# Performance work log

Measured on AMD Instinct MI355X. Metric: run time of the kernel, lower is better.

## Reference

```python
import jax, jax.numpy as jnp
import numpy as np

N_NODES = 50000
N_EDGES = 800000
N_FEAT = 128
HIDDEN = 256
N_CLASSES = 40
K_HOPS = 10
ALPHA = 0.1


def setup_inputs() -> dict:
    key = jax.random.key(0)
    k1, k2, k3, k4 = jax.random.split(key, 4)
    x = jax.random.normal(k1, (N_NODES, N_FEAT), dtype=jnp.float32)
    edge_index = jax.random.randint(k2, (2, N_EDGES), 0, N_NODES, dtype=jnp.int64)
    # PPR init of gamma weights: temp[k] = alpha*(1-alpha)^k, temp[K] = (1-alpha)^K
    temp_np = ALPHA * (1.0 - ALPHA) ** np.arange(K_HOPS + 1)
    temp_np[-1] = (1.0 - ALPHA) ** K_HOPS
    temp = jnp.asarray(temp_np, dtype=jnp.float32)
    W1 = jax.random.normal(k3, (N_FEAT, HIDDEN), dtype=jnp.float32) * (1.0 / np.sqrt(N_FEAT))
    b1 = jnp.zeros((HIDDEN,), dtype=jnp.float32)
    W2 = jax.random.normal(k4, (HIDDEN, N_CLASSES), dtype=jnp.float32) * (1.0 / np.sqrt(HIDDEN))
    b2 = jnp.zeros((N_CLASSES,), dtype=jnp.float32)
    return {"x": x, "edge_index": edge_index, "temp": temp,
            "W1": W1, "b1": b1, "W2": W2, "b2": b2, "K": K_HOPS}


def reference(x, edge_index, temp, W1, b1, W2, b2, K):
    N = x.shape[0]
    # gcn_norm with self-loops (fill value 1): A_hat = D^-1/2 (A + I) D^-1/2
    loops = jnp.arange(N, dtype=edge_index.dtype)
    row = jnp.concatenate([edge_index[0], loops])  # source (x_j)
    col = jnp.concatenate([edge_index[1], loops])  # target (aggregation)
    ones = jnp.ones(row.shape[0], dtype=x.dtype)
    deg = jax.ops.segment_sum(ones, col, num_segments=N)
    dinv = jnp.where(deg > 0, deg ** -0.5, jnp.zeros_like(deg))
    norm = dinv[row] * dinv[col]  # [E+N]

    # K-hop propagation with learned hop-weighted sum
    h = x
    hidden = temp[0] * x
    for k in range(K):  # small fixed hop count
        msg = norm[:, None] * h[row]                      # gather + scale
        h = jax.ops.segment_sum(msg, col, num_segments=N)  # scatter-add
        hidden = hidden + temp[k + 1] * h

    # eval mode: dropout is a no-op
    z = jax.nn.relu(hidden @ W1 + b1)
    z = z @ W2 + b2
    return jax.nn.log_softmax(z, axis=1)
```

## Files before the change

### kernel.cpp

```cpp
#include <hip/hip_runtime.h>
#include <hip/hip_bf16.h>


#define NFEAT 128
#define HID   256
#define NCLS  40
#define KHOPS 10

typedef __attribute__((ext_vector_type(8))) short short8;
typedef __attribute__((ext_vector_type(4))) float floatx4;

__device__ __forceinline__ float blo(unsigned g) { return __uint_as_float(g << 16); }
__device__ __forceinline__ float bhi(unsigned g) { return __uint_as_float(g & 0xffff0000u); }
__device__ __forceinline__ unsigned f2bf(float x) {
  unsigned u = __float_as_uint(x);
  return (u + 0x7fffu + ((u >> 16) & 1u)) >> 16;
}
__device__ __forceinline__ unsigned bpack(float a, float b) {
  return f2bf(a) | (f2bf(b) << 16);
}

__global__ void k_detect64(const unsigned int* __restrict__ raw, int* __restrict__ flag) {
  __shared__ int any;
  int t = threadIdx.x;
  if (t == 0) any = 0;
  __syncthreads();
  if (raw[2 * t + 1] != 0u) any = 1;
  __syncthreads();
  if (t == 0) flag[0] = (any == 0) ? 1 : 0;
}

__global__ void k_zero(int* __restrict__ p, int n) {
  int i = blockIdx.x * blockDim.x + threadIdx.x;
  if (i < n) p[i] = 0;
}

__global__ void k_count(const int* __restrict__ ei32, const long long* __restrict__ ei64,
                        int E, int N, int* __restrict__ cnt, int* __restrict__ rank,
                        const int* __restrict__ flag) {
  int e = blockIdx.x * blockDim.x + threadIdx.x;
  if (e >= E) return;
  int dst = flag[0] ? (int)ei64[(size_t)E + e] : ei32[(size_t)E + e];
  if ((unsigned)dst < (unsigned)N) rank[e] = atomicAdd(&cnt[dst], 1);
  else rank[e] = -1;
}

__global__ __launch_bounds__(256) void k_scan_a(
    const int* __restrict__ cnt, int* __restrict__ bsum, int n) {
  int t = threadIdx.x;
  int base = blockIdx.x * 1024 + t * 4;
  int s = 0;
  if (base + 3 < n) {
    int4 v = *(const int4*)(cnt + base);
    s = v.x + v.y + v.z + v.w;
  } else {
    #pragma unroll
    for (int j = 0; j < 4; ++j) if (base + j < n) s += cnt[base + j];
  }
  #pragma unroll
  for (int off = 1; off < 64; off <<= 1) s += __shfl_xor(s, off);
  __shared__ int ws[4];
  if ((t & 63) == 0) ws[t >> 6] = s;
  __syncthreads();
  if (t == 0) bsum[blockIdx.x] = ws[0] + ws[1] + ws[2] + ws[3];
}

__global__ void k_scan_mid(int* __restrict__ bsum, int* __restrict__ S,
                           int ntiles, int n) {
  int t = threadIdx.x;
  int lane = t & 63, wid = t >> 6;
  int v = (t < ntiles) ? bsum[t] : 0;
  int x = v;
  #pragma unroll
  for (int off = 1; off < 64; off <<= 1) {
    int u = __shfl_up(x, off);
    if (lane >= off) x += u;
  }
  __shared__ int ws[16];
  if (lane == 63) ws[wid] = x;
  __syncthreads();
  if (wid == 0) {
    int s2 = (lane < 16) ? ws[lane] : 0;
    #pragma unroll
    for (int off = 1; off < 16; off <<= 1) {
      int u = __shfl_up(s2, off);
      if (lane >= off) s2 += u;
    }
    if (lane < 16) ws[lane] = s2;
  }
  __syncthreads();
  int woff = wid ? ws[wid - 1] : 0;
  if (t < ntiles) bsum[t] = x - v + woff;
  if (t == 0) S[n] = ws[15];
}

__global__ __launch_bounds__(256) void k_scan_c(
    const int* __restrict__ cnt, const int* __restrict__ bsum,
    int* __restrict__ S, float* __restrict__ dinv, int n) {
  int t = threadIdx.x;
  int base = blockIdx.x * 1024 + t * 4;
  int v[4];
  if (base + 3 < n) {
    int4 q = *(const int4*)(cnt + base);
    v[0] = q.x; v[1] = q.y; v[2] = q.z; v[3] = q.w;
  } else {
    #pragma unroll
    for (int j = 0; j < 4; ++j) v[j] = (base + j < n) ? cnt[base + j] : 0;
  }
  int tsum = v[0] + v[1] + v[2] + v[3];
  int lane = t & 63, wv = t >> 6;
  int x = tsum;
  #pragma unroll
  for (int off = 1; off < 64; off <<= 1) {
    int u = __shfl_up(x, off);
    if (lane >= off) x += u;
  }
  __shared__ int ws[4];
  if (lane == 63) ws[wv] = x;
  __syncthreads();
  int woff = 0;
  #pragma unroll
  for (int j = 0; j < 4; ++j) if (j < wv) woff += ws[j];
  int run = x - tsum + woff + bsum[blockIdx.x];
  #pragma unroll
  for (int j = 0; j < 4; ++j) {
    int idx = base + j;
    if (idx < n) {
      S[idx] = run;
      dinv[idx] = rsqrtf((float)(v[j] + 1));
      run += v[j];
    }
  }
}

__global__ void k_fill(const int* __restrict__ ei32, const long long* __restrict__ ei64,
                       int E, int N, const int* __restrict__ S,
                       const int* __restrict__ rank, int* __restrict__ csr,
                       const int* __restrict__ flag) {
  int e = blockIdx.x * blockDim.x + threadIdx.x;
  if (e >= E) return;
  int r = rank[e];
  if (r < 0) return;
  int src, dst;
  if (flag[0]) { src = (int)ei64[e]; dst = (int)ei64[(size_t)E + e]; }
  else         { src = ei32[e];      dst = ei32[(size_t)E + e]; }
  if ((unsigned)src >= (unsigned)N) return;
  csr[S[dst] + r] = src;
}

__global__ void k_init(const float* __restrict__ x, const float* __restrict__ dinv,
                       unsigned* __restrict__ p0, int total64) {
  int i = blockIdx.x * blockDim.x + threadIdx.x;
  if (i >= total64) return;
  float2 xv = ((const float2*)x)[i];
  float di = dinv[i >> 6];
  p0[i] = bpack(di * xv.x, di * xv.y);
}

__global__ __launch_bounds__(256) void k_prop(
    const unsigned* __restrict__ pin, unsigned* __restrict__ pout,
    const int* __restrict__ S, const int* __restrict__ csr,
    const float* __restrict__ dinv, int N) {
  int wid = __builtin_amdgcn_readfirstlane(threadIdx.x >> 6);
  int lane = threadIdx.x & 63;
  int node = blockIdx.x * 4 + wid;
  if (node >= N) return;
  int g = lane & 15;
  int e = lane >> 4;
  int s = S[node], en = S[node + 1];
  float acc[8] = {0.f, 0.f, 0.f, 0.f, 0.f, 0.f, 0.f, 0.f};
  for (int p = s; p < en; p += 16) {
    uint4 gd[4];
    float wt[4];
    #pragma unroll
    for (int t = 0; t < 4; ++t) {
      int pj = p + t * 4 + e;
      int sidx = csr[pj < en ? pj : s];
      wt[t] = (pj < en) ? 1.f : 0.f;
      gd[t] = *(const uint4*)(pin + (size_t)sidx * 64 + g * 4);
    }
    #pragma unroll
    for (int t = 0; t < 4; ++t) {
      const unsigned* gu = (const unsigned*)&gd[t];
      #pragma unroll
      for (int u = 0; u < 4; ++u) {
        acc[u * 2]     += wt[t] * blo(gu[u]);
        acc[u * 2 + 1] += wt[t] * bhi(gu[u]);
      }
    }
  }
  #pragma unroll
  for (int u = 0; u < 8; ++u) {
    acc[u] += __shfl_xor(acc[u], 16);
    acc[u] += __shfl_xor(acc[u], 32);
  }
  if (e == 0) {
    float di = dinv[node];
    float dd = di * di;
    uint4 gs = *(const uint4*)(pin + (size_t)node * 64 + g * 4);
    const unsigned* su = (const unsigned*)&gs;
    #pragma unroll
    for (int u = 0; u < 4; ++u) {
      acc[u * 2]     += blo(su[u]);
      acc[u * 2 + 1] += bhi(su[u]);
    }
    uint4 pk;
    pk.x = bpack(dd * acc[0], dd * acc[1]);
    pk.y = bpack(dd * acc[2], dd * acc[3]);
    pk.z = bpack(dd * acc[4], dd * acc[5]);
    pk.w = bpack(dd * acc[6], dd * acc[7]);
    *(uint4*)(pout + (size_t)node * 64 + g * 4) = pk;
  }
}

__global__ __launch_bounds__(256) void k_gemm1f(
    const unsigned* __restrict__ pbuf, const float* __restrict__ temp,
    const float* __restrict__ dinv, const float* __restrict__ W1,
    const float* __restrict__ b1, unsigned short* __restrict__ z1, int M) {
  __shared__ unsigned short As[64][136];
  __shared__ unsigned short Bs[16][128][8];
  int tid = threadIdx.x;
  int m0 = blockIdx.x * 64;
  size_t slab = (size_t)M * 64;
  float tk[KHOPS + 1];
  #pragma unroll
  for (int k = 0; k <= KHOPS; ++k) tk[k] = temp[k];
  for (int idx = tid; idx < 64 * 16; idx += 256) {
    int m = idx >> 4, c = idx & 15;
    int row = m0 + m; if (row >= M) row = M - 1;
    const unsigned* pp = pbuf + (size_t)row * 64 + c * 4;
    float tL[4] = {0.f, 0.f, 0.f, 0.f}, tH[4] = {0.f, 0.f, 0.f, 0.f};
    #pragma unroll
    for (int k = 0; k <= KHOPS; ++k) {
      uint4 v = *(const uint4*)(pp + slab * k);
      const unsigned* vu = (const unsigned*)&v;
      #pragma unroll
      for (int u = 0; u < 4; ++u) {
        tL[u] += tk[k] * blo(vu[u]);
        tH[u] += tk[k] * bhi(vu[u]);
      }
    }
    float inv = 1.f / dinv[row];
    uint4 o;
    o.x = bpack(tL[0] * inv, tH[0] * inv);
    o.y = bpack(tL[1] * inv, tH[1] * inv);
    o.z = bpack(tL[2] * inv, tH[2] * inv);
    o.w = bpack(tL[3] * inv, tH[3] * inv);
    *(uint4*)&As[m][c * 8] = o;
  }
  __syncthreads();
  int lane = tid & 63;
  int q = lane >> 4, r16 = lane & 15;
  int nw = (tid >> 6) * 32;
  #pragma unroll
  for (int pass = 0; pass < 2; ++pass) {
    int n0 = pass * 128;
    if (pass) __syncthreads();
    for (int idx = tid; idx < 128 * 128; idx += 256) {
      int k = idx >> 7, n = idx & 127;
      Bs[k >> 3][n][k & 7] = (unsigned short)f2bf(W1[(size_t)k * HID + n0 + n]);
    }
    __syncthreads();
    floatx4 acc[4][2] = {};
    #pragma unroll
    for (int step = 0; step < 4; ++step) {
      int k0 = step * 32;
      short8 a[4], b[2];
      #pragma unroll
      for (int i = 0; i < 4; ++i)
        a[i] = *(const short8*)&As[i * 16 + r16][k0 + q * 8];
      #pragma unroll
      for (int j = 0; j < 2; ++j)
        b[j] = *(const short8*)&Bs[step * 4 + q][nw + j * 16 + r16][0];
      #pragma unroll
      for (int i = 0; i < 4; ++i)
        #pragma unroll
        for (int j = 0; j < 2; ++j)
          acc[i][j] = __builtin_amdgcn_mfma_f32_16x16x32_bf16(a[i], b[j], acc[i][j], 0, 0, 0);
    }
    __syncthreads();
    unsigned short* Zs = &Bs[0][0][0];
    #pragma unroll
    for (int j = 0; j < 2; ++j) {
      int n = nw + j * 16 + r16;
      float bias = b1[n0 + n];
      #pragma unroll
      for (int i = 0; i < 4; ++i) {
        #pragma unroll
        for (int r = 0; r < 4; ++r) {
          int m = i * 16 + q * 4 + r;
          float v = fmaxf(acc[i][j][r] + bias, 0.f);
          Zs[m * 136 + n] = (unsigned short)f2bf(v);
        }
      }
    }
    __syncthreads();
    for (int idx = tid; idx < 64 * 16; idx += 256) {
      int m = idx >> 4, c = idx & 15;
      int row = m0 + m;
      if (row < M) {
        uint4 v = *(const uint4*)&Zs[m * 136 + c * 8];
        *(uint4*)(z1 + (size_t)row * HID + n0 + c * 8) = v;
      }
    }
  }
}

__global__ void k_w2prep(const float* __restrict__ W2, unsigned short* __restrict__ W2t) {
  int i = blockIdx.x * blockDim.x + threadIdx.x;
  if (i >= 48 * 256) return;
  int n = i >> 8, k = i & 255;
  W2t[n * 256 + k] = (n < NCLS) ? (unsigned short)f2bf(W2[(size_t)k * NCLS + n]) : 0;
}

__global__ __launch_bounds__(256) void k_mlp2(
    const unsigned short* __restrict__ z1, const unsigned short* __restrict__ W2t,
    const float* __restrict__ b2, float* __restrict__ out, int N) {
  int tid = threadIdx.x;
  int lane = tid & 63;
  int wv = tid >> 6;
  int node0 = blockIdx.x * 64 + wv * 16;
  int q = lane >> 4, m = lane & 15;
  int arow = node0 + m; if (arow >= N) arow = N - 1;
  const unsigned short* aptr = z1 + (size_t)arow * HID + q * 8;
  const unsigned short* bptr = W2t + (size_t)m * HID + q * 8;
  floatx4 acc[3] = {};
  #pragma unroll
  for (int step = 0; step < 8; ++step) {
    short8 a = *(const short8*)(aptr + step * 32);
    #pragma unroll
    for (int j = 0; j < 3; ++j) {
      short8 b = *(const short8*)(bptr + (size_t)j * 16 * HID + step * 32);
      acc[j] = __builtin_amdgcn_mfma_f32_16x16x32_bf16(a, b, acc[j], 0, 0, 0);
    }
  }
  int c = m;
  bool v2 = (c < NCLS - 32);
  float bb0 = b2[c], bb1 = b2[c + 16];
  float bb2 = v2 ? b2[c + 32] : 0.f;
  #pragma unroll
  for (int r = 0; r < 4; ++r) {
    int node = node0 + q * 4 + r;
    float l0 = acc[0][r] + bb0;
    float l1 = acc[1][r] + bb1;
    float l2 = v2 ? (acc[2][r] + bb2) : -3.4e38f;
    float mx = fmaxf(fmaxf(l0, l1), l2);
    #pragma unroll
    for (int off = 1; off < 16; off <<= 1) mx = fmaxf(mx, __shfl_xor(mx, off));
    float sm = __expf(l0 - mx) + __expf(l1 - mx) + (v2 ? __expf(l2 - mx) : 0.f);
    #pragma unroll
    for (int off = 1; off < 16; off <<= 1) sm += __shfl_xor(sm, off);
    float lse = mx + __logf(sm);
    if (node < N) {
      float* op = out + (size_t)node * NCLS + c;
      op[0] = l0 - lse;
      op[16] = l1 - lse;
      if (v2) op[32] = l2 - lse;
    }
  }
}

extern "C" void kernel_launch(void* const* d_in, const int* in_sizes, int n_in,
                              void* d_out, int out_size, void* d_ws, size_t ws_size,
                              hipStream_t stream) {
  const float*     x    = (const float*)d_in[0];
  const int*       ei32 = (const int*)d_in[1];
  const long long* ei64 = (const long long*)d_in[1];
  const float*     temp = (const float*)d_in[2];
  const float*     W1   = (const float*)d_in[3];
  const float*     b1   = (const float*)d_in[4];
  const float*     W2   = (const float*)d_in[5];
  const float*     b2   = (const float*)d_in[6];
  float* out = (float*)d_out;

  int N = in_sizes[0] / NFEAT;
  int E = in_sizes[1] / 2;

  char* w = (char*)d_ws;
  auto carve = [&](size_t bytes) -> void* {
    void* p = (void*)w;
    w += (bytes + 255) & ~(size_t)255;
    return p;
  };
  int*      flag      = (int*)     carve(4);
  int*      cnt       = (int*)     carve((size_t)N * 4);
  int*      S         = (int*)     carve(((size_t)N + 1) * 4);
  float*    dinv      = (float*)   carve((size_t)N * 4);
  int*      bsum      = (int*)     carve(1024 * 4);
  unsigned short* W2t = (unsigned short*)carve(48 * 256 * 2);
  int*      rank      = (int*)     carve((size_t)E * 4);
  int*      csr       = (int*)     carve((size_t)E * 4);
  unsigned* pbuf      = (unsigned*)carve((size_t)(KHOPS + 1) * N * 64 * 4);
  unsigned short* z1  = (unsigned short*)carve((size_t)N * HID * 2);

  int ntiles = (N + 1023) / 1024;
  size_t slab = (size_t)N * 64;

  k_detect64<<<1, 256, 0, stream>>>((const unsigned int*)d_in[1], flag);
  k_zero<<<(N + 255) / 256, 256, 0, stream>>>(cnt, N);
  k_count<<<(E + 255) / 256, 256, 0, stream>>>(ei32, ei64, E, N, cnt, rank, flag);
  k_scan_a<<<ntiles, 256, 0, stream>>>(cnt, bsum, N);
  k_scan_mid<<<1, 1024, 0, stream>>>(bsum, S, ntiles, N);
  k_scan_c<<<ntiles, 256, 0, stream>>>(cnt, bsum, S, dinv, N);
  k_fill<<<(E + 255) / 256, 256, 0, stream>>>(ei32, ei64, E, N, S, rank, csr, flag);
  k_init<<<(N * 64 + 255) / 256, 256, 0, stream>>>(x, dinv, pbuf, N * 64);
  k_w2prep<<<48, 256, 0, stream>>>(W2, W2t);

  for (int k = 0; k < KHOPS; ++k) {
    k_prop<<<(N + 3) / 4, 256, 0, stream>>>(
        pbuf + slab * k, pbuf + slab * (k + 1), S, csr, dinv, N);
  }

  k_gemm1f<<<(N + 63) / 64, 256, 0, stream>>>(
      pbuf, temp, dinv, W1, b1, z1, N);
  k_mlp2<<<(N + 63) / 64, 256, 0, stream>>>(z1, W2t, b2, out, N);
}
```

Before: 488.9 us.

## Fuse hop-sum, first GEMM, second GEMM and log-softmax into one kernel

Merges the hop-weighted sum plus W1 GEMM kernel with the W2 GEMM and log-softmax kernel, so the bf16 hidden activations stay in shared memory and are never written to or reread from global memory. W1 is converted to transposed bf16 once in a new prep kernel. Each block no longer re-converts all of W1 into LDS; MFMA B operands now come straight from global W1t, with each wave covering 64 output columns in a single pass. The trade-off is more accumulator registers per thread, a declared occupancy target of 4 blocks, and B loads that depend on cache instead of LDS.

```diff
diff --git a/kernel.cpp b/kernel.cpp
--- a/kernel.cpp
+++ b/kernel.cpp
@@ -213,18 +213,33 @@
   }
 }
 
-__global__ __launch_bounds__(256) void k_gemm1f(
+__global__ void k_w1prep(const float* __restrict__ W1, unsigned short* __restrict__ W1t) {
+  int i = blockIdx.x * blockDim.x + threadIdx.x;
+  if (i >= 256 * 128) return;
+  int n = i >> 7, k = i & 127;
+  W1t[n * 128 + k] = (unsigned short)f2bf(W1[(size_t)k * HID + n]);
+}
+
+__global__ void k_w2prep(const float* __restrict__ W2, unsigned short* __restrict__ W2t) {
+  int i = blockIdx.x * blockDim.x + threadIdx.x;
+  if (i >= 48 * 256) return;
+  int n = i >> 8, k = i & 255;
+  W2t[n * 256 + k] = (n < NCLS) ? (unsigned short)f2bf(W2[(size_t)k * NCLS + n]) : 0;
+}
+
+__global__ __launch_bounds__(256, 4) void k_fused(
     const unsigned* __restrict__ pbuf, const float* __restrict__ temp,
-    const float* __restrict__ dinv, const float* __restrict__ W1,
-    const float* __restrict__ b1, unsigned short* __restrict__ z1, int M) {
-  __shared__ unsigned short As[64][136];
-  __shared__ unsigned short Bs[16][128][8];
+    const float* __restrict__ dinv, const unsigned short* __restrict__ W1t,
+    const float* __restrict__ b1, const unsigned short* __restrict__ W2t,
+    const float* __restrict__ b2, float* __restrict__ out, int M) {
+  __shared__ unsigned short sbuf[64 * 264];
   int tid = threadIdx.x;
   int m0 = blockIdx.x * 64;
   size_t slab = (size_t)M * 64;
   float tk[KHOPS + 1];
   #pragma unroll
   for (int k = 0; k <= KHOPS; ++k) tk[k] = temp[k];
+
   for (int idx = tid; idx < 64 * 16; idx += 256) {
     int m = idx >> 4, c = idx & 15;
     int row = m0 + m; if (row >= M) row = M - 1;
@@ -246,104 +261,73 @@
     o.y = bpack(tL[1] * inv, tH[1] * inv);
     o.z = bpack(tL[2] * inv, tH[2] * inv);
     o.w = bpack(tL[3] * inv, tH[3] * inv);
-    *(uint4*)&As[m][c * 8] = o;
-  }
-  __syncthreads();
-  int lane = tid & 63;
-  int q = lane >> 4, r16 = lane & 15;
-  int nw = (tid >> 6) * 32;
-  #pragma unroll
-  for (int pass = 0; pass < 2; ++pass) {
-    int n0 = pass * 128;
-    if (pass) __syncthreads();
-    for (int idx = tid; idx < 128 * 128; idx += 256) {
-      int k = idx >> 7, n = idx & 127;
-      Bs[k >> 3][n][k & 7] = (unsigned short)f2bf(W1[(size_t)k * HID + n0 + n]);
-    }
-    __syncthreads();
-    floatx4 acc[4][2] = {};
-    #pragma unroll
-    for (int step = 0; step < 4; ++step) {
-      int k0 = step * 32;
-      short8 a[4], b[2];
-      #pragma unroll
-      for (int i = 0; i < 4; ++i)
-        a[i] = *(const short8*)&As[i * 16 + r16][k0 + q * 8];
-      #pragma unroll
-      for (int j = 0; j < 2; ++j)
-        b[j] = *(const short8*)&Bs[step * 4 + q][nw + j * 16 + r16][0];
-      #pragma unroll
-      for (int i = 0; i < 4; ++i)
-        #pragma unroll
-        for (int j = 0; j < 2; ++j)
-          acc[i][j] = __builtin_amdgcn_mfma_f32_16x16x32_bf16(a[i], b[j], acc[i][j], 0, 0, 0);
-    }
-    __syncthreads();
-    unsigned short* Zs = &Bs[0][0][0];
-    #pragma unroll
-    for (int j = 0; j < 2; ++j) {
-      int n = nw + j * 16 + r16;
-      float bias = b1[n0 + n];
-      #pragma unroll
-      for (int i = 0; i < 4; ++i) {
-        #pragma unroll
-        for (int r = 0; r < 4; ++r) {
-          int m = i * 16 + q * 4 + r;
-          float v = fmaxf(acc[i][j][r] + bias, 0.f);
-          Zs[m * 136 + n] = (unsigned short)f2bf(v);
-        }
-      }
-    }
-    __syncthreads();
-    for (int idx = tid; idx < 64 * 16; idx += 256) {
-      int m = idx >> 4, c = idx & 15;
-      int row = m0 + m;
-      if (row < M) {
-        uint4 v = *(const uint4*)&Zs[m * 136 + c * 8];
-        *(uint4*)(z1 + (size_t)row * HID + n0 + c * 8) = v;
-      }
-    }
-  }
-}
-
-__global__ void k_w2prep(const float* __restrict__ W2, unsigned short* __restrict__ W2t) {
-  int i = blockIdx.x * blockDim.x + threadIdx.x;
-  if (i >= 48 * 256) return;
-  int n = i >> 8, k = i & 255;
-  W2t[n * 256 + k] = (n < NCLS) ? (unsigned short)f2bf(W2[(size_t)k * NCLS + n]) : 0;
-}
-
-__global__ __launch_bounds__(256) void k_mlp2(
-    const unsigned short* __restrict__ z1, const unsigned short* __restrict__ W2t,
-    const float* __restrict__ b2, float* __restrict__ out, int N) {
-  int tid = threadIdx.x;
+    *(uint4*)&sbuf[m * 136 + c * 8] = o;
+  }
+  __syncthreads();
+
   int lane = tid & 63;
   int wv = tid >> 6;
-  int node0 = blockIdx.x * 64 + wv * 16;
-  int q = lane >> 4, m = lane & 15;
-  int arow = node0 + m; if (arow >= N) arow = N - 1;
-  const unsigned short* aptr = z1 + (size_t)arow * HID + q * 8;
-  const unsigned short* bptr = W2t + (size_t)m * HID + q * 8;
-  floatx4 acc[3] = {};
+  int q = lane >> 4, r16 = lane & 15;
+
+  floatx4 acc[4][4] = {};
+  #pragma unroll
+  for (int step = 0; step < 4; ++step) {
+    int k0 = step * 32;
+    short8 a[4], b[4];
+    #pragma unroll
+    for (int i = 0; i < 4; ++i)
+      a[i] = *(const short8*)&sbuf[(i * 16 + r16) * 136 + k0 + q * 8];
+    #pragma unroll
+    for (int j = 0; j < 4; ++j)
+      b[j] = *(const short8*)&W1t[(size_t)(wv * 64 + j * 16 + r16) * 128 + k0 + q * 8];
+    #pragma unroll
+    for (int i = 0; i < 4; ++i)
+      #pragma unroll
+      for (int j = 0; j < 4; ++j)
+        acc[i][j] = __builtin_amdgcn_mfma_f32_16x16x32_bf16(a[i], b[j], acc[i][j], 0, 0, 0);
+  }
+  __syncthreads();
+
+  #pragma unroll
+  for (int j = 0; j < 4; ++j) {
+    int n = wv * 64 + j * 16 + r16;
+    float bias = b1[n];
+    #pragma unroll
+    for (int i = 0; i < 4; ++i) {
+      #pragma unroll
+      for (int r = 0; r < 4; ++r) {
+        int m = i * 16 + q * 4 + r;
+        float v = fmaxf(acc[i][j][r] + bias, 0.f);
+        sbuf[m * 264 + n] = (unsigned short)f2bf(v);
+      }
+    }
+  }
+  __syncthreads();
+
+  int node0 = m0 + wv * 16;
+  int mm = lane & 15;
+  const unsigned short* aL = &sbuf[(wv * 16 + mm) * 264 + q * 8];
+  const unsigned short* bptr = W2t + (size_t)mm * HID + q * 8;
+  floatx4 acc2[3] = {};
   #pragma unroll
   for (int step = 0; step < 8; ++step) {
-    short8 a = *(const short8*)(aptr + step * 32);
+    short8 a = *(const short8*)(aL + step * 32);
     #pragma unroll
     for (int j = 0; j < 3; ++j) {
       short8 b = *(const short8*)(bptr + (size_t)j * 16 * HID + step * 32);
-      acc[j] = __builtin_amdgcn_mfma_f32_16x16x32_bf16(a, b, acc[j], 0, 0, 0);
-    }
-  }
-  int c = m;
+      acc2[j] = __builtin_amdgcn_mfma_f32_16x16x32_bf16(a, b, acc2[j], 0, 0, 0);
+    }
+  }
+  int c = mm;
   bool v2 = (c < NCLS - 32);
   float bb0 = b2[c], bb1 = b2[c + 16];
   float bb2 = v2 ? b2[c + 32] : 0.f;
   #pragma unroll
   for (int r = 0; r < 4; ++r) {
     int node = node0 + q * 4 + r;
-    float l0 = acc[0][r] + bb0;
-    float l1 = acc[1][r] + bb1;
-    float l2 = v2 ? (acc[2][r] + bb2) : -3.4e38f;
+    float l0 = acc2[0][r] + bb0;
+    float l1 = acc2[1][r] + bb1;
+    float l2 = v2 ? (acc2[2][r] + bb2) : -3.4e38f;
     float mx = fmaxf(fmaxf(l0, l1), l2);
     #pragma unroll
     for (int off = 1; off < 16; off <<= 1) mx = fmaxf(mx, __shfl_xor(mx, off));
@@ -351,7 +335,7 @@
     #pragma unroll
     for (int off = 1; off < 16; off <<= 1) sm += __shfl_xor(sm, off);
     float lse = mx + __logf(sm);
-    if (node < N) {
+    if (node < M) {
       float* op = out + (size_t)node * NCLS + c;
       op[0] = l0 - lse;
       op[16] = l1 - lse;
@@ -387,11 +371,11 @@
   int*      S         = (int*)     carve(((size_t)N + 1) * 4);
   float*    dinv      = (float*)   carve((size_t)N * 4);
   int*      bsum      = (int*)     carve(1024 * 4);
+  unsigned short* W1t = (unsigned short*)carve(256 * 128 * 2);
   unsigned short* W2t = (unsigned short*)carve(48 * 256 * 2);
   int*      rank      = (int*)     carve((size_t)E * 4);
   int*      csr       = (int*)     carve((size_t)E * 4);
   unsigned* pbuf      = (unsigned*)carve((size_t)(KHOPS + 1) * N * 64 * 4);
-  unsigned short* z1  = (unsigned short*)carve((size_t)N * HID * 2);
 
   int ntiles = (N + 1023) / 1024;
   size_t slab = (size_t)N * 64;
@@ -404,6 +388,7 @@
   k_scan_c<<<ntiles, 256, 0, stream>>>(cnt, bsum, S, dinv, N);
   k_fill<<<(E + 255) / 256, 256, 0, stream>>>(ei32, ei64, E, N, S, rank, csr, flag);
   k_init<<<(N * 64 + 255) / 256, 256, 0, stream>>>(x, dinv, pbuf, N * 64);
+  k_w1prep<<<128, 256, 0, stream>>>(W1, W1t);
   k_w2prep<<<48, 256, 0, stream>>>(W2, W2t);
 
   for (int k = 0; k < KHOPS; ++k) {
@@ -411,7 +396,6 @@
         pbuf + slab * k, pbuf + slab * (k + 1), S, csr, dinv, N);
   }
 
-  k_gemm1f<<<(N + 63) / 64, 256, 0, stream>>>(
-      pbuf, temp, dinv, W1, b1, z1, N);
-  k_mlp2<<<(N + 63) / 64, 256, 0, stream>>>(z1, W2t, b2, out, N);
-}
+  k_fused<<<(N + 63) / 64, 256, 0, stream>>>(
+      pbuf, temp, dinv, W1t, b1, W2t, b2, out, N);
+}
```

Result: faster. 473.5 us (-3.2%).
